# Kernel optimization log

Hardware: AMD Instinct MI355X
Metric: run time of the kernel (lower is better)

Reference implementation:

```python
import jax, jax.numpy as jnp
import numpy as np

GRID = 1024  # grid resolution -> V = GRID*GRID vertices


def _grid_mesh(G):
    """Build a triangulated GxG grid mesh; return laplacian directed edges and
    normal-consistency interior-edge index quadruples [v0, v1, v2, v3] where
    (v0,v1) is the shared edge and v2, v3 the opposite vertices of the two faces."""
    V = G * G
    i, j = np.meshgrid(np.arange(G - 1), np.arange(G - 1), indexing="ij")
    a = (i * G + j).ravel(); b = (i * G + j + 1).ravel()
    c = ((i + 1) * G + j).ravel(); d = ((i + 1) * G + j + 1).ravel()
    faces = np.concatenate([np.stack([a, b, c], 1), np.stack([b, d, c], 1)], 0).astype(np.int64)
    # half-edges with opposite vertex per face
    e = np.concatenate([faces[:, [0, 1]], faces[:, [1, 2]], faces[:, [2, 0]]], 0)
    opp = np.concatenate([faces[:, 2], faces[:, 0], faces[:, 1]], 0)
    e = np.sort(e, 1)
    key = e[:, 0] * V + e[:, 1]
    order = np.argsort(key, kind="stable")
    ks, opps = key[order], opp[order]
    dup = np.nonzero(ks[1:] == ks[:-1])[0]  # edges shared by exactly two faces
    nc_idx = np.stack([ks[dup] // V, ks[dup] % V, opps[dup], opps[dup + 1]], 1)
    uk = np.unique(key)
    src, dst = uk // V, uk % V
    lap_src = np.concatenate([src, dst])
    lap_dst = np.concatenate([dst, src])
    return lap_src.astype(np.int32), lap_dst.astype(np.int32), nc_idx.astype(np.int32)


def setup_inputs() -> dict:
    key = jax.random.key(0)
    k1, k2 = jax.random.split(key)
    G = GRID; V = G * G
    lap_src, lap_dst, nc_idx = _grid_mesh(G)
    verts = jax.random.normal(k1, (V, 3), jnp.float32)          # template_mesh.verts_packed()
    deform_verts = jax.random.normal(k2, (V, 3), jnp.float32) * 0.05  # nn.Parameter
    return {
        "verts": verts,
        "deform_verts": deform_verts,
        "lap_src": jnp.asarray(lap_src),
        "lap_dst": jnp.asarray(lap_dst),
        "nc_idx": jnp.asarray(nc_idx),
        "batch_size": 4,
    }


def reference(verts, deform_verts, lap_src, lap_dst, nc_idx, batch_size):
    V = verts.shape[0]
    new_verts = verts + deform_verts  # Meshes.offset_verts

    # mesh_laplacian_smoothing(method='uniform'):
    # per-vertex (mean of neighbors - vertex), loss = mean ||.||
    nbr_sum = jax.ops.segment_sum(new_verts[lap_src], lap_dst, num_segments=V)
    deg = jax.ops.segment_sum(jnp.ones(lap_src.shape, jnp.float32), lap_dst, num_segments=V)
    lap = nbr_sum / jnp.maximum(deg, 1.0)[:, None] - new_verts
    laplacian_loss = jnp.linalg.norm(lap, axis=1).mean()

    # mesh_normal_consistency: for each interior edge (v0,v1) with opposite
    # verts v2, v3: n0 = (v1-v0) x (v2-v0), n1 = -(v1-v0) x (v3-v0),
    # loss = mean(1 - cos(n0, n1))
    v0 = new_verts[nc_idx[:, 0]]; v1 = new_verts[nc_idx[:, 1]]
    v2 = new_verts[nc_idx[:, 2]]; v3 = new_verts[nc_idx[:, 3]]
    e01 = v1 - v0
    n0 = jnp.cross(e01, v2 - v0)
    n1 = -jnp.cross(e01, v3 - v0)
    cos = (n0 * n1).sum(-1) / jnp.maximum(
        jnp.linalg.norm(n0, axis=-1) * jnp.linalg.norm(n1, axis=-1), 1e-8)
    flatten_loss = (1.0 - cos).mean()

    # Meshes.extend(batch_size): replicate deformed mesh verts
    batched_verts = jnp.broadcast_to(new_verts, (batch_size, V, 3))
    return batched_verts, laplacian_loss, flatten_loss
```

## Files before the change

### kernel.cpp

```cpp
#include <hip/hip_runtime.h>

#define G 1024
#define ROWF 3072
#define ROWF4 768
#define V (G * G)
#define NBLK 1024
#define COPY4 786432
#define NEDGE 3137541.0f

typedef float v4 __attribute__((ext_vector_type(4)));

struct F3 { float x, y, z; };

__device__ inline F3 ldl(const float* __restrict__ nv, int slot, int col) {
    int b = slot * ROWF + 3 * col;
    F3 r; r.x = nv[b]; r.y = nv[b + 1]; r.z = nv[b + 2];
    return r;
}

__device__ inline float omc(F3 v0, F3 v1, F3 v2, F3 v3) {
    float ex = v1.x - v0.x, ey = v1.y - v0.y, ez = v1.z - v0.z;
    float ax = v2.x - v0.x, ay = v2.y - v0.y, az = v2.z - v0.z;
    float bx = v3.x - v0.x, by = v3.y - v0.y, bz = v3.z - v0.z;
    float n0x = ey * az - ez * ay;
    float n0y = ez * ax - ex * az;
    float n0z = ex * ay - ey * ax;
    float n1x = ez * by - ey * bz;
    float n1y = ex * bz - ez * bx;
    float n1z = ey * bx - ex * by;
    float dd = n0x * n1x + n0y * n1y + n0z * n1z;
    float m0 = sqrtf(n0x * n0x + n0y * n0y + n0z * n0z);
    float m1 = sqrtf(n1x * n1x + n1y * n1y + n1z * n1z);
    float c  = dd / fmaxf(m0 * m1, 1e-8f);
    return 1.0f - c;
}

__global__ __launch_bounds__(256) void fused_kernel(const float* __restrict__ verts,
                                                    const float* __restrict__ dv,
                                                    float* __restrict__ out,
                                                    float* __restrict__ wsp) {
    int b = blockIdx.x;
    int i = ((b & 7) << 7) | (b >> 3);
    int t = threadIdx.x;

    __shared__ v4 nv4[3 * ROWF4];
    const float* nv = (const float*)nv4;

    const v4* vin4 = (const v4*)verts;
    const v4* dvi4 = (const v4*)dv;

    #pragma unroll
    for (int s = 0; s < 3; ++s) {
        int r = i + s - 1;
        r = r < 0 ? 0 : (r > G - 1 ? G - 1 : r);
        int base = r * ROWF4;
        #pragma unroll
        for (int k = 0; k < 3; ++k) {
            int idx = t + (k << 8);
            nv4[s * ROWF4 + idx] = vin4[base + idx] + dvi4[base + idx];
        }
    }
    __syncthreads();

    bool hasU = (i > 0), hasD = (i < G - 1);

    v4* out4 = (v4*)out;
    #pragma unroll
    for (int k = 0; k < 3; ++k) {
        int idx = t + (k << 8);
        v4 val  = nv4[ROWF4 + idx];
        int oi  = i * ROWF4 + idx;
        __builtin_nontemporal_store(val, &out4[oi]);
        __builtin_nontemporal_store(val, &out4[oi + COPY4]);
        __builtin_nontemporal_store(val, &out4[oi + 2 * COPY4]);
        __builtin_nontemporal_store(val, &out4[oi + 3 * COPY4]);
    }

    float lap_sum = 0.0f, fl_sum = 0.0f;

    #pragma unroll
    for (int k = 0; k < 4; ++k) {
        int j = t + (k << 8);
        bool hasL = (j > 0), hasR = (j < G - 1);

        F3 self = ldl(nv, 1, j);
        F3 pL{0,0,0}, pR{0,0,0}, pU{0,0,0}, pD{0,0,0}, pUR{0,0,0}, pDL{0,0,0}, pDR{0,0,0};
        if (hasL)          pL  = ldl(nv, 1, j - 1);
        if (hasR)          pR  = ldl(nv, 1, j + 1);
        if (hasU)          pU  = ldl(nv, 0, j);
        if (hasD)          pD  = ldl(nv, 2, j);
        if (hasU && hasR)  pUR = ldl(nv, 0, j + 1);
        if (hasD && hasL)  pDL = ldl(nv, 2, j - 1);
        if (hasD && hasR)  pDR = ldl(nv, 2, j + 1);

        int   degi = (int)hasL + (int)hasR + (int)hasU + (int)hasD
                   + (int)(hasU && hasR) + (int)(hasD && hasL);
        float inv  = 1.0f / (float)degi;
        float lx = (pL.x + pR.x + pU.x + pD.x + pUR.x + pDL.x) * inv - self.x;
        float ly = (pL.y + pR.y + pU.y + pD.y + pUR.y + pDL.y) * inv - self.y;
        float lz = (pL.z + pR.z + pU.z + pD.z + pUR.z + pDL.z) * inv - self.z;
        lap_sum += sqrtf(lx * lx + ly * ly + lz * lz);

        if (hasD && hasR) {
            fl_sum += omc(pR, pD, self, pDR);
            if (hasU) fl_sum += omc(self, pR, pD, pUR);
            if (hasL) fl_sum += omc(self, pD, pR, pDL);
        }
    }

    for (int off = 32; off > 0; off >>= 1) {
        lap_sum += __shfl_down(lap_sum, off);
        fl_sum  += __shfl_down(fl_sum, off);
    }
    __shared__ float red[8];
    int lane = t & 63, wv = t >> 6;
    if (lane == 0) { red[wv] = lap_sum; red[4 + wv] = fl_sum; }
    __syncthreads();
    if (t == 0) {
        wsp[b]        = red[0] + red[1] + red[2] + red[3];
        wsp[NBLK + b] = red[4] + red[5] + red[6] + red[7];
    }
}

__global__ __launch_bounds__(256) void finalize_kernel(const float* __restrict__ wsp,
                                                       float* __restrict__ out) {
    float s = 0.0f, f = 0.0f;
    for (int k = threadIdx.x; k < NBLK; k += 256) {
        s += wsp[k];
        f += wsp[NBLK + k];
    }
    for (int off = 32; off > 0; off >>= 1) {
        s += __shfl_down(s, off);
        f += __shfl_down(f, off);
    }
    __shared__ float red[8];
    int lane = threadIdx.x & 63, wv = threadIdx.x >> 6;
    if (lane == 0) { red[wv] = s; red[4 + wv] = f; }
    __syncthreads();
    if (threadIdx.x == 0) {
        out[12 * V]     = (red[0] + red[1] + red[2] + red[3]) / (float)V;
        out[12 * V + 1] = (red[4] + red[5] + red[6] + red[7]) / NEDGE;
    }
}

extern "C" void kernel_launch(void* const* d_in, const int* in_sizes, int n_in,
                              void* d_out, int out_size, void* d_ws, size_t ws_size,
                              hipStream_t stream) {
    const float* verts = (const float*)d_in[0];
    const float* dv    = (const float*)d_in[1];
    float* out = (float*)d_out;
    float* wsp = (float*)d_ws;

    fused_kernel<<<NBLK, 256, 0, stream>>>(verts, dv, out, wsp);
    finalize_kernel<<<1, 256, 0, stream>>>(wsp, out);
}
```

Baseline: 154.2 us.

## Process two grid rows per block to cut halo reloads and fuse output stores

Each block now handles two rows with 512 threads and stages four rows in shared memory instead of three per row, which cuts redundant halo row loads from global memory from 3x to 2x. The broadcast output stores are issued straight from the load loop for the two interior rows, so they no longer go through a second shared-memory read. The cost is fewer, larger blocks (512 instead of 1024) with more shared memory each, and an integer divide in the load index math. Per-block partial sums now go into a 512-entry workspace that the finalize kernel reduces.

```diff
diff --git a/kernel.cpp b/kernel.cpp
--- a/kernel.cpp
+++ b/kernel.cpp
@@ -4,7 +4,7 @@
 #define ROWF 3072
 #define ROWF4 768
 #define V (G * G)
-#define NBLK 1024
+#define NBLK 512
 #define COPY4 786432
 #define NEDGE 3137541.0f
 
@@ -35,63 +35,60 @@
     return 1.0f - c;
 }
 
-__global__ __launch_bounds__(256) void fused_kernel(const float* __restrict__ verts,
+__global__ __launch_bounds__(512) void fused_kernel(const float* __restrict__ verts,
                                                     const float* __restrict__ dv,
                                                     float* __restrict__ out,
                                                     float* __restrict__ wsp) {
-    int b = blockIdx.x;
-    int i = ((b & 7) << 7) | (b >> 3);
-    int t = threadIdx.x;
+    int b  = blockIdx.x;
+    int i0 = (((b & 7) << 6) | (b >> 3)) << 1;
+    int t  = threadIdx.x;
 
-    __shared__ v4 nv4[3 * ROWF4];
+    __shared__ v4 nv4[4 * ROWF4];
     const float* nv = (const float*)nv4;
 
     const v4* vin4 = (const v4*)verts;
     const v4* dvi4 = (const v4*)dv;
+    v4* out4 = (v4*)out;
 
     #pragma unroll
-    for (int s = 0; s < 3; ++s) {
-        int r = i + s - 1;
+    for (int m = 0; m < 6; ++m) {
+        int flat = t + (m << 9);
+        int s    = flat / ROWF4;
+        int c    = flat - s * ROWF4;
+        int r    = i0 - 1 + s;
         r = r < 0 ? 0 : (r > G - 1 ? G - 1 : r);
-        int base = r * ROWF4;
-        #pragma unroll
-        for (int k = 0; k < 3; ++k) {
-            int idx = t + (k << 8);
-            nv4[s * ROWF4 + idx] = vin4[base + idx] + dvi4[base + idx];
+        v4 val = vin4[r * ROWF4 + c] + dvi4[r * ROWF4 + c];
+        nv4[flat] = val;
+        if (flat >= ROWF4 && flat < 3 * ROWF4) {
+            int oi = (i0 - 1 + s) * ROWF4 + c;
+            __builtin_nontemporal_store(val, &out4[oi]);
+            __builtin_nontemporal_store(val, &out4[oi + COPY4]);
+            __builtin_nontemporal_store(val, &out4[oi + 2 * COPY4]);
+            __builtin_nontemporal_store(val, &out4[oi + 3 * COPY4]);
         }
     }
     __syncthreads();
 
-    bool hasU = (i > 0), hasD = (i < G - 1);
-
-    v4* out4 = (v4*)out;
-    #pragma unroll
-    for (int k = 0; k < 3; ++k) {
-        int idx = t + (k << 8);
-        v4 val  = nv4[ROWF4 + idx];
-        int oi  = i * ROWF4 + idx;
-        __builtin_nontemporal_store(val, &out4[oi]);
-        __builtin_nontemporal_store(val, &out4[oi + COPY4]);
-        __builtin_nontemporal_store(val, &out4[oi + 2 * COPY4]);
-        __builtin_nontemporal_store(val, &out4[oi + 3 * COPY4]);
-    }
+    int r  = t >> 8;
+    int gi = i0 + r;
+    int sc = r + 1;
+    bool hasU = (gi > 0), hasD = (gi < G - 1);
 
     float lap_sum = 0.0f, fl_sum = 0.0f;
-
     #pragma unroll
     for (int k = 0; k < 4; ++k) {
-        int j = t + (k << 8);
+        int j = (t & 255) + (k << 8);
         bool hasL = (j > 0), hasR = (j < G - 1);
 
-        F3 self = ldl(nv, 1, j);
+        F3 self = ldl(nv, sc, j);
         F3 pL{0,0,0}, pR{0,0,0}, pU{0,0,0}, pD{0,0,0}, pUR{0,0,0}, pDL{0,0,0}, pDR{0,0,0};
-        if (hasL)          pL  = ldl(nv, 1, j - 1);
-        if (hasR)          pR  = ldl(nv, 1, j + 1);
-        if (hasU)          pU  = ldl(nv, 0, j);
-        if (hasD)          pD  = ldl(nv, 2, j);
-        if (hasU && hasR)  pUR = ldl(nv, 0, j + 1);
-        if (hasD && hasL)  pDL = ldl(nv, 2, j - 1);
-        if (hasD && hasR)  pDR = ldl(nv, 2, j + 1);
+        if (hasL)          pL  = ldl(nv, sc,     j - 1);
+        if (hasR)          pR  = ldl(nv, sc,     j + 1);
+        if (hasU)          pU  = ldl(nv, sc - 1, j);
+        if (hasD)          pD  = ldl(nv, sc + 1, j);
+        if (hasU && hasR)  pUR = ldl(nv, sc - 1, j + 1);
+        if (hasD && hasL)  pDL = ldl(nv, sc + 1, j - 1);
+        if (hasD && hasR)  pDR = ldl(nv, sc + 1, j + 1);
 
         int   degi = (int)hasL + (int)hasR + (int)hasU + (int)hasD
                    + (int)(hasU && hasR) + (int)(hasD && hasL);
@@ -112,13 +109,16 @@
         lap_sum += __shfl_down(lap_sum, off);
         fl_sum  += __shfl_down(fl_sum, off);
     }
-    __shared__ float red[8];
+    __shared__ float red[16];
     int lane = t & 63, wv = t >> 6;
-    if (lane == 0) { red[wv] = lap_sum; red[4 + wv] = fl_sum; }
+    if (lane == 0) { red[wv] = lap_sum; red[8 + wv] = fl_sum; }
     __syncthreads();
     if (t == 0) {
-        wsp[b]        = red[0] + red[1] + red[2] + red[3];
-        wsp[NBLK + b] = red[4] + red[5] + red[6] + red[7];
+        float ls = 0.0f, fs = 0.0f;
+        #pragma unroll
+        for (int w = 0; w < 8; ++w) { ls += red[w]; fs += red[8 + w]; }
+        wsp[b]        = ls;
+        wsp[NBLK + b] = fs;
     }
 }
 
@@ -151,6 +151,6 @@
     float* out = (float*)d_out;
     float* wsp = (float*)d_ws;
 
-    fused_kernel<<<NBLK, 256, 0, stream>>>(verts, dv, out, wsp);
+    fused_kernel<<<NBLK, 512, 0, stream>>>(verts, dv, out, wsp);
     finalize_kernel<<<1, 256, 0, stream>>>(wsp, out);
 }
```

New measurement: 159.4 us. +3.4%, slower.
